# Kernel optimization log

Measured on AMD Instinct MI355X. Metric: run time of the kernel, lower is better.

The kernel has to match this reference:

```python
import jax, jax.numpy as jnp
import numpy as np

N, E = 8000, 128000
IN_DIM = OUT_DIM = REL_DIM = 64
NUM_RELS, NUM_BASES = 200, 50
R2 = 2 * NUM_RELS


def setup_inputs() -> dict:
    key = jax.random.key(0)
    ks = jax.random.split(key, 10)
    feat = jax.random.normal(ks[0], (N, IN_DIM), jnp.float32)
    rel_emb = jax.random.normal(ks[1], (R2, REL_DIM), jnp.float32)
    weight = jax.random.normal(ks[2], (NUM_BASES, IN_DIM, OUT_DIM), jnp.float32) * 0.05
    w_comp = jax.random.normal(ks[3], (R2, NUM_BASES), jnp.float32) * 0.1
    self_loop_weight = jax.random.normal(ks[4], (IN_DIM, OUT_DIM), jnp.float32) * 0.05
    W_R_w = jax.random.normal(ks[5], (REL_DIM, REL_DIM), jnp.float32) * 0.05
    W_R_b = jnp.zeros((REL_DIM,), jnp.float32)
    src = jax.random.randint(ks[6], (E,), 0, N, dtype=jnp.int32)
    dst = jax.random.randint(ks[7], (E,), 0, N, dtype=jnp.int32)
    etype = jax.random.randint(ks[8], (E,), 0, R2, dtype=jnp.int32)
    return dict(feat=feat, rel_emb=rel_emb, weight=weight, w_comp=w_comp,
                self_loop_weight=self_loop_weight, W_R_w=W_R_w, W_R_b=W_R_b,
                src=src, dst=dst, etype=etype)


def reference(feat, rel_emb, weight, w_comp, self_loop_weight, W_R_w, W_R_b,
              src, dst, etype):
    # rel_weight = (w_comp @ weight.view(B, in*out)).view(R2, in, out)
    rel_weight = jnp.einsum('rb,bio->rio', w_comp, weight)          # [R2, in, out]
    # msg_func: per-edge relation weight gather + bmm (gather-mm pattern)
    w_e = rel_weight[etype]                                          # [E, in, out]
    msg = jnp.einsum('ei,eio->eo', feat[src], w_e)                   # [E, out]
    # aggregator: alpha = 1/in_deg(dst) per edge -> weighted sum == mean over mailbox
    ones = jnp.ones((msg.shape[0],), msg.dtype)
    in_deg = jax.ops.segment_sum(ones, dst, num_segments=N)          # [N]
    nei_sum = jax.ops.segment_sum(msg, dst, num_segments=N)          # [N, out]
    nei_msg = nei_sum / jnp.maximum(in_deg, 1.0)[:, None]
    # curr_emb = dst_feat @ self_loop_weight (same for every edge into a node)
    curr_emb = feat @ self_loop_weight                               # [N, out]
    h = curr_emb + nei_msg                                           # no bias / no activation
    # is_input_layer=True: repr = cat([feat, h])
    repr_ = jnp.concatenate([feat, h], axis=1)                       # [N, in+out]
    # edge_update: W_R linear on relation embeddings (act is None)
    rel_emb_new = rel_emb @ W_R_w.T + W_R_b                          # [R2, rel_dim]
    return repr_, rel_emb_new
```

## Files before the change

### kernel.cpp

```cpp
#include <hip/hip_runtime.h>

#define N_NODES 8000
#define E_EDGES 128000
#define NUM_BASES 50
#define R2 400
#define CPR 8
#define RT 16
#define HB 32
#define EPB (E_EDGES / HB)

static __device__ __forceinline__ float bf2f(unsigned short u) {
    return __uint_as_float(((unsigned int)u) << 16);
}
static __device__ __forceinline__ unsigned short f2bf(float f) {
    unsigned int u = __float_as_uint(f);
    u += 0x7fffu + ((u >> 16) & 1u);
    return (unsigned short)(u >> 16);
}
static __device__ __forceinline__ float bcast(float v, int lane) {
    return __uint_as_float(__builtin_amdgcn_readlane(__float_as_uint(v), lane));
}

__global__ __launch_bounds__(256) void k_zero(int4* __restrict__ p, int n4) {
    const int i = blockIdx.x * 256 + threadIdx.x;
    if (i < n4) p[i] = make_int4(0, 0, 0, 0);
}

__global__ __launch_bounds__(256) void k_pre(const float* __restrict__ w_comp,
                                             const float* __restrict__ weight,
                                             unsigned short* __restrict__ relWh,
                                             const int* __restrict__ dst,
                                             const int* __restrict__ etype,
                                             int* __restrict__ bcnt,
                                             int* __restrict__ dcnt16) {
    const int blk = blockIdx.x;
    const int t = threadIdx.x;
    if (blk < 100) {
        const int rt = blk >> 2;
        const int pb = blk & 3;
        const int r0 = rt * RT;
        const int p = pb * 256 + t;
        const float4* w4 = (const float4*)weight;
        float4 acc[RT];
#pragma unroll
        for (int rr = 0; rr < RT; ++rr) acc[rr] = make_float4(0.f, 0.f, 0.f, 0.f);
        for (int b = 0; b < NUM_BASES; ++b) {
            const float4 w = w4[b * 1024 + p];
#pragma unroll
            for (int rr = 0; rr < RT; ++rr) {
                const float c = w_comp[(r0 + rr) * NUM_BASES + b];
                acc[rr].x = fmaf(c, w.x, acc[rr].x);
                acc[rr].y = fmaf(c, w.y, acc[rr].y);
                acc[rr].z = fmaf(c, w.z, acc[rr].z);
                acc[rr].w = fmaf(c, w.w, acc[rr].w);
            }
        }
        ushort4* outh = (ushort4*)relWh;
#pragma unroll
        for (int rr = 0; rr < RT; ++rr) {
            ushort4 v;
            v.x = f2bf(acc[rr].x); v.y = f2bf(acc[rr].y);
            v.z = f2bf(acc[rr].z); v.w = f2bf(acc[rr].w);
            outh[(r0 + rr) * 1024 + p] = v;
        }
    } else {
        __shared__ int lcnt[R2];
        const int hb = blk - 100;
        for (int i = t; i < R2; i += 256) lcnt[i] = 0;
        __syncthreads();
        const int e0 = hb * EPB;
        for (int e = e0 + t; e < e0 + EPB; e += 256) {
            atomicAdd(&lcnt[etype[e]], 1);
            atomicAdd(&dcnt16[dst[e] * 16], 1);
        }
        __syncthreads();
        for (int i = t; i < R2; i += 256) bcnt[hb * R2 + i] = lcnt[i];
    }
}

__global__ __launch_bounds__(512) void k_scan(const int* __restrict__ bcnt,
                                              const int* __restrict__ dcnt16,
                                              int* __restrict__ off,
                                              int* __restrict__ doff,
                                              int* __restrict__ bbase,
                                              int* __restrict__ dcursor16) {
    __shared__ int sh[8];
    const int t = threadIdx.x;
    const int lane = t & 63;
    const int wid = t >> 6;
    if (blockIdx.x == 0) {
        int tot = 0;
        if (t < R2)
            for (int b = 0; b < HB; ++b) tot += bcnt[b * R2 + t];
        int v = tot;
#pragma unroll
        for (int d = 1; d < 64; d <<= 1) {
            const int u = __shfl_up(v, d, 64);
            if (lane >= d) v += u;
        }
        if (lane == 63) sh[wid] = v;
        __syncthreads();
        int wo = 0;
        for (int i = 0; i < wid; ++i) wo += sh[i];
        const int incl = v + wo;
        const int ex = incl - tot;
        if (t == 0) off[0] = 0;
        if (t < R2) {
            off[t + 1] = incl;
            int run = ex;
            for (int b = 0; b < HB; ++b) {
                bbase[b * R2 + t] = run;
                run += bcnt[b * R2 + t];
            }
        }
    } else {
        int loc[32];
        int run = 0;
        const int base = t * 32;
        if (t < 256) {
#pragma unroll
            for (int q = 0; q < 32; ++q) {
                const int v = (base + q < N_NODES) ? dcnt16[(base + q) * 16] : 0;
                loc[q] = run;
                run += v;
            }
        }
        int v = (t < 256) ? run : 0;
#pragma unroll
        for (int d = 1; d < 64; d <<= 1) {
            const int u = __shfl_up(v, d, 64);
            if (lane >= d) v += u;
        }
        if (lane == 63 && wid < 4) sh[wid] = v;
        __syncthreads();
        if (t < 256) {
            int wo = 0;
            for (int i = 0; i < wid; ++i) wo += sh[i];
            const int incl = v + wo;
            const int ex = incl - run;
#pragma unroll
            for (int q = 0; q < 32; ++q) {
                if (base + q < N_NODES) {
                    const int o = ex + loc[q];
                    doff[base + q] = o;
                    dcursor16[(base + q) * 16] = o;
                }
            }
            if (t == 255) doff[N_NODES] = incl;
        }
    }
}

__global__ __launch_bounds__(256) void k_scatter(const int* __restrict__ src,
                                                 const int* __restrict__ dst,
                                                 const int* __restrict__ etype,
                                                 const int* __restrict__ bbase,
                                                 int* __restrict__ dcursor16,
                                                 int2* __restrict__ sedge) {
    __shared__ int lcur[R2];
    const int blk = blockIdx.x;
    const int t = threadIdx.x;
    for (int i = t; i < R2; i += 256) lcur[i] = bbase[blk * R2 + i];
    __syncthreads();
    const int e0 = blk * EPB;
    for (int e = e0 + t; e < e0 + EPB; e += 256) {
        const int r = etype[e];
        const int d = dst[e];
        const int rpos = atomicAdd(&lcur[r], 1);
        const int dpos = atomicAdd(&dcursor16[d * 16], 1);
        sedge[rpos] = make_int2(src[e], dpos);
    }
}

__global__ __launch_bounds__(64, 1) void k_edge(const float* __restrict__ feat,
                                                const unsigned short* __restrict__ relWh,
                                                const int2* __restrict__ sedge,
                                                const int* __restrict__ off,
                                                unsigned short* __restrict__ msg) {
    const int blk = blockIdx.x;
    const int xcd = blk & 7;
    const int j = blk >> 3;
    const int r = xcd * 50 + (j >> 3);
    const int chunk = j & 7;
    const int lane = threadIdx.x;
    const int beg = off[r];
    const int cnt = off[r + 1] - beg;
    const int cbeg = beg + (cnt * chunk) / CPR;
    const int cend = beg + (cnt * (chunk + 1)) / CPR;

    const unsigned short* __restrict__ Wh = relWh + r * 4096;
    float w[64];
#pragma unroll
    for (int i = 0; i < 64; ++i) w[i] = bf2f(Wh[i * 64 + lane]);

    int idx = cbeg;
    for (; idx + 1 < cend; idx += 2) {
        const int2 eA = sedge[idx];
        const int2 eB = sedge[idx + 1];
        const int sA = __builtin_amdgcn_readfirstlane(eA.x);
        const int dA = __builtin_amdgcn_readfirstlane(eA.y);
        const int sB = __builtin_amdgcn_readfirstlane(eB.x);
        const int dB = __builtin_amdgcn_readfirstlane(eB.y);
        const float* __restrict__ fA = feat + sA * 64;
        const float* __restrict__ fB = feat + sB * 64;
        float a0 = 0.f, a1 = 0.f, a2 = 0.f, a3 = 0.f;
        float b0 = 0.f, b1 = 0.f, b2 = 0.f, b3 = 0.f;
#pragma unroll
        for (int i = 0; i < 64; i += 4) {
            a0 = fmaf(fA[i    ], w[i    ], a0);  b0 = fmaf(fB[i    ], w[i    ], b0);
            a1 = fmaf(fA[i + 1], w[i + 1], a1);  b1 = fmaf(fB[i + 1], w[i + 1], b1);
            a2 = fmaf(fA[i + 2], w[i + 2], a2);  b2 = fmaf(fB[i + 2], w[i + 2], b2);
            a3 = fmaf(fA[i + 3], w[i + 3], a3);  b3 = fmaf(fB[i + 3], w[i + 3], b3);
        }
        msg[dA * 64 + lane] = f2bf((a0 + a1) + (a2 + a3));
        msg[dB * 64 + lane] = f2bf((b0 + b1) + (b2 + b3));
    }
    if (idx < cend) {
        const int2 eA = sedge[idx];
        const int sA = __builtin_amdgcn_readfirstlane(eA.x);
        const int dA = __builtin_amdgcn_readfirstlane(eA.y);
        const float* __restrict__ frow = feat + sA * 64;
        float a0 = 0.f, a1 = 0.f, a2 = 0.f, a3 = 0.f;
#pragma unroll
        for (int i = 0; i < 64; i += 4) {
            a0 = fmaf(frow[i    ], w[i    ], a0);
            a1 = fmaf(frow[i + 1], w[i + 1], a1);
            a2 = fmaf(frow[i + 2], w[i + 2], a2);
            a3 = fmaf(frow[i + 3], w[i + 3], a3);
        }
        msg[dA * 64 + lane] = f2bf((a0 + a1) + (a2 + a3));
    }
}

__global__ __launch_bounds__(256) void k_post(const float* __restrict__ feat,
                                              const float* __restrict__ slw,
                                              const int* __restrict__ doff,
                                              const unsigned short* __restrict__ msg,
                                              const float* __restrict__ rel_emb,
                                              const float* __restrict__ Wr,
                                              const float* __restrict__ br,
                                              float* __restrict__ out) {
    __shared__ float s_w[4096];
    const int blk = blockIdx.x;
    const int t = threadIdx.x;
    const int lane = t & 63;
    const int wv = t >> 6;
    if (blk < 500) {
#pragma unroll
        for (int k = 0; k < 16; ++k) s_w[k * 256 + t] = slw[k * 256 + t];
        __syncthreads();
#pragma unroll
        for (int q = 0; q < 4; ++q) {
            const int n = blk * 16 + wv * 4 + q;
            const int b0 = doff[n];
            const int b1 = doff[n + 1];
            const float* __restrict__ frow = feat + n * 64;
            const float fa = frow[lane];
            float acc = 0.f;
#pragma unroll
            for (int i = 0; i < 64; ++i)
                acc = fmaf(frow[i], s_w[i * 64 + lane], acc);
            float sm = 0.f;
            int jj = b0;
            for (; jj + 3 < b1; jj += 4) {
                const float m0 = bf2f(msg[jj * 64 + lane]);
                const float m1 = bf2f(msg[(jj + 1) * 64 + lane]);
                const float m2 = bf2f(msg[(jj + 2) * 64 + lane]);
                const float m3 = bf2f(msg[(jj + 3) * 64 + lane]);
                sm += (m0 + m1) + (m2 + m3);
            }
            for (; jj < b1; ++jj) sm += bf2f(msg[jj * 64 + lane]);
            const float inv = 1.0f / fmaxf((float)(b1 - b0), 1.0f);
            out[n * 128 + lane] = fa;
            out[n * 128 + 64 + lane] = fmaf(sm, inv, acc);
        }
    } else {
#pragma unroll
        for (int k = 0; k < 16; ++k) {
            const int idx = k * 256 + t;
            s_w[(idx & 63) * 64 + (idx >> 6)] = Wr[idx];
        }
        __syncthreads();
        const int r = (blk - 500) * 4 + wv;
        const float re = rel_emb[r * 64 + lane];
        float acc = br[lane];
#pragma unroll
        for (int k = 0; k < 64; ++k)
            acc = fmaf(bcast(re, k), s_w[k * 64 + lane], acc);
        out[N_NODES * 128 + r * 64 + lane] = acc;
    }
}

extern "C" void kernel_launch(void* const* d_in, const int* in_sizes, int n_in,
                              void* d_out, int out_size, void* d_ws, size_t ws_size,
                              hipStream_t stream) {
    const float* feat    = (const float*)d_in[0];
    const float* rel_emb = (const float*)d_in[1];
    const float* weight  = (const float*)d_in[2];
    const float* w_comp  = (const float*)d_in[3];
    const float* slw     = (const float*)d_in[4];
    const float* Wr      = (const float*)d_in[5];
    const float* br      = (const float*)d_in[6];
    const int*   src     = (const int*)d_in[7];
    const int*   dst     = (const int*)d_in[8];
    const int*   etype   = (const int*)d_in[9];
    float* out = (float*)d_out;
    char* ws = (char*)d_ws;

    unsigned short* relWh   = (unsigned short*)(ws);
    unsigned short* msg     = (unsigned short*)(ws + 3276800);
    int2* sedge     = (int2*)(ws + 19660800);
    int* off        = (int*)(ws + 20684800);
    int* doff       = (int*)(ws + 20686464);
    int* bcnt       = (int*)(ws + 20718528);
    int* bbase      = (int*)(ws + 20769728);
    int* dcnt16     = (int*)(ws + 20820928);
    int* dcursor16  = (int*)(ws + 21332928);

    k_zero<<<125, 256, 0, stream>>>((int4*)dcnt16, 32000);
    k_pre<<<132, 256, 0, stream>>>(w_comp, weight, relWh, dst, etype,
                                   bcnt, dcnt16);
    k_scan<<<2, 512, 0, stream>>>(bcnt, dcnt16, off, doff, bbase, dcursor16);
    k_scatter<<<HB, 256, 0, stream>>>(src, dst, etype, bbase, dcursor16, sedge);
    k_edge<<<R2 * CPR, 64, 0, stream>>>(feat, relWh, sedge, off, msg);
    k_post<<<600, 256, 0, stream>>>(feat, slw, doff, msg, rel_emb, Wr, br, out);
}
```

Before: 117.1 us.

## Replace global dst-count atomics with per-block shared histograms and parallel scan

Destination in-degree counting and the cursor used for placing edges into dst-sorted order now run on per-block shared-memory histograms (64 blocks × 8000 nodes) instead of padded global atomics. The zero-fill kernel is removed. The single-block node scan becomes a 250-block scan that uses a global atomic cursor to hand out node bases, so node segments are laid out in arbitrary order, with per-node counts stored explicitly for the post kernel. This targets global atomic contention and the serial scan bottleneck, at the cost of more workspace traffic for the 64×8000 count and base arrays.

```diff
diff --git a/kernel.cpp b/kernel.cpp
--- a/kernel.cpp
+++ b/kernel.cpp
@@ -4,10 +4,10 @@
 #define E_EDGES 128000
 #define NUM_BASES 50
 #define R2 400
+#define HB 64
+#define EPB (E_EDGES / HB)
+#define RT 16
 #define CPR 8
-#define RT 16
-#define HB 32
-#define EPB (E_EDGES / HB)
 
 static __device__ __forceinline__ float bf2f(unsigned short u) {
     return __uint_as_float(((unsigned int)u) << 16);
@@ -16,14 +16,6 @@
     unsigned int u = __float_as_uint(f);
     u += 0x7fffu + ((u >> 16) & 1u);
     return (unsigned short)(u >> 16);
-}
-static __device__ __forceinline__ float bcast(float v, int lane) {
-    return __uint_as_float(__builtin_amdgcn_readlane(__float_as_uint(v), lane));
-}
-
-__global__ __launch_bounds__(256) void k_zero(int4* __restrict__ p, int n4) {
-    const int i = blockIdx.x * 256 + threadIdx.x;
-    if (i < n4) p[i] = make_int4(0, 0, 0, 0);
 }
 
 __global__ __launch_bounds__(256) void k_pre(const float* __restrict__ w_comp,
@@ -32,10 +24,13 @@
                                              const int* __restrict__ dst,
                                              const int* __restrict__ etype,
                                              int* __restrict__ bcnt,
-                                             int* __restrict__ dcnt16) {
+                                             int* __restrict__ dbcnt,
+                                             int* __restrict__ gcur) {
+    __shared__ int lcnt[8400];
     const int blk = blockIdx.x;
     const int t = threadIdx.x;
     if (blk < 100) {
+        if (blk == 0 && t == 0) gcur[0] = 0;
         const int rt = blk >> 2;
         const int pb = blk & 3;
         const int r0 = rt * RT;
@@ -64,89 +59,95 @@
             outh[(r0 + rr) * 1024 + p] = v;
         }
     } else {
-        __shared__ int lcnt[R2];
-        const int hb = blk - 100;
-        for (int i = t; i < R2; i += 256) lcnt[i] = 0;
-        __syncthreads();
-        const int e0 = hb * EPB;
+        const int h = blk - 100;
+        for (int i = t; i < 8400; i += 256) lcnt[i] = 0;
+        __syncthreads();
+        const int e0 = h * EPB;
         for (int e = e0 + t; e < e0 + EPB; e += 256) {
-            atomicAdd(&lcnt[etype[e]], 1);
-            atomicAdd(&dcnt16[dst[e] * 16], 1);
-        }
-        __syncthreads();
-        for (int i = t; i < R2; i += 256) bcnt[hb * R2 + i] = lcnt[i];
-    }
-}
-
-__global__ __launch_bounds__(512) void k_scan(const int* __restrict__ bcnt,
-                                              const int* __restrict__ dcnt16,
+            atomicAdd(&lcnt[dst[e]], 1);
+            atomicAdd(&lcnt[8000 + etype[e]], 1);
+        }
+        __syncthreads();
+        for (int i = t; i < 8000; i += 256) dbcnt[h * 8000 + i] = lcnt[i];
+        for (int i = t; i < 400; i += 256) bcnt[h * 400 + i] = lcnt[8000 + i];
+    }
+}
+
+__global__ __launch_bounds__(256) void k_scan(const int* __restrict__ bcnt,
+                                              const int* __restrict__ dbcnt,
                                               int* __restrict__ off,
                                               int* __restrict__ doff,
+                                              int* __restrict__ dtot,
                                               int* __restrict__ bbase,
-                                              int* __restrict__ dcursor16) {
-    __shared__ int sh[8];
+                                              int* __restrict__ dbase,
+                                              int* __restrict__ gcur) {
     const int t = threadIdx.x;
     const int lane = t & 63;
-    const int wid = t >> 6;
-    if (blockIdx.x == 0) {
+    const int wv = t >> 6;
+    if (blockIdx.x < 250) {
+        __shared__ int T[64 * 32];
+        __shared__ int sdoff[32];
+        __shared__ int sbase;
+        const int n0 = blockIdx.x * 32;
+#pragma unroll
+        for (int pass = 0; pass < 8; ++pass) {
+            const int row = pass * 8 + (t >> 5);
+            const int col = t & 31;
+            T[row * 32 + col] = dbcnt[row * 8000 + n0 + col];
+        }
+        __syncthreads();
         int tot = 0;
-        if (t < R2)
-            for (int b = 0; b < HB; ++b) tot += bcnt[b * R2 + t];
-        int v = tot;
-#pragma unroll
-        for (int d = 1; d < 64; d <<= 1) {
-            const int u = __shfl_up(v, d, 64);
-            if (lane >= d) v += u;
-        }
-        if (lane == 63) sh[wid] = v;
-        __syncthreads();
-        int wo = 0;
-        for (int i = 0; i < wid; ++i) wo += sh[i];
-        const int incl = v + wo;
-        const int ex = incl - tot;
-        if (t == 0) off[0] = 0;
-        if (t < R2) {
-            off[t + 1] = incl;
-            int run = ex;
-            for (int b = 0; b < HB; ++b) {
-                bbase[b * R2 + t] = run;
-                run += bcnt[b * R2 + t];
-            }
+        if (t < 32) {
+            for (int hb = 0; hb < 64; ++hb) tot += T[hb * 32 + t];
+        }
+        int v = (t < 64) ? tot : 0;
+        if (t < 64) {
+#pragma unroll
+            for (int d = 1; d < 64; d <<= 1) {
+                const int u = __shfl_up(v, d, 64);
+                if (lane >= d) v += u;
+            }
+        }
+        if (t == 31) sbase = atomicAdd(gcur, v);
+        __syncthreads();
+        if (t < 32) {
+            const int dn = sbase + v - tot;
+            doff[n0 + t] = dn;
+            dtot[n0 + t] = tot;
+            sdoff[t] = dn;
+        }
+        __syncthreads();
+        for (int nl = wv; nl < 32; nl += 4) {
+            const int orig = T[lane * 32 + nl];
+            int s = orig;
+#pragma unroll
+            for (int d = 1; d < 64; d <<= 1) {
+                const int u = __shfl_up(s, d, 64);
+                if (lane >= d) s += u;
+            }
+            dbase[lane * 8000 + n0 + nl] = sdoff[nl] + s - orig;
         }
     } else {
-        int loc[32];
-        int run = 0;
-        const int base = t * 32;
-        if (t < 256) {
-#pragma unroll
-            for (int q = 0; q < 32; ++q) {
-                const int v = (base + q < N_NODES) ? dcnt16[(base + q) * 16] : 0;
-                loc[q] = run;
-                run += v;
-            }
-        }
-        int v = (t < 256) ? run : 0;
-#pragma unroll
-        for (int d = 1; d < 64; d <<= 1) {
-            const int u = __shfl_up(v, d, 64);
-            if (lane >= d) v += u;
-        }
-        if (lane == 63 && wid < 4) sh[wid] = v;
-        __syncthreads();
-        if (t < 256) {
-            int wo = 0;
-            for (int i = 0; i < wid; ++i) wo += sh[i];
-            const int incl = v + wo;
-            const int ex = incl - run;
-#pragma unroll
-            for (int q = 0; q < 32; ++q) {
-                if (base + q < N_NODES) {
-                    const int o = ex + loc[q];
-                    doff[base + q] = o;
-                    dcursor16[(base + q) * 16] = o;
-                }
-            }
-            if (t == 255) doff[N_NODES] = incl;
+        __shared__ int s[800];
+        for (int r = t; r < 400; r += 256) {
+            int sum = 0;
+            for (int hb = 0; hb < HB; ++hb) sum += bcnt[hb * 400 + r];
+            s[r] = sum;
+        }
+        __syncthreads();
+        if (t == 0) {
+            int run = 0;
+            for (int r = 0; r < 400; ++r) { s[400 + r] = run; run += s[r]; }
+            off[0] = 0;
+        }
+        __syncthreads();
+        for (int r = t; r < 400; r += 256) {
+            int run = s[400 + r];
+            off[r + 1] = run + s[r];
+            for (int hb = 0; hb < HB; ++hb) {
+                bbase[hb * 400 + r] = run;
+                run += bcnt[hb * 400 + r];
+            }
         }
     }
 }
@@ -155,19 +156,20 @@
                                                  const int* __restrict__ dst,
                                                  const int* __restrict__ etype,
                                                  const int* __restrict__ bbase,
-                                                 int* __restrict__ dcursor16,
+                                                 const int* __restrict__ dbase,
                                                  int2* __restrict__ sedge) {
-    __shared__ int lcur[R2];
-    const int blk = blockIdx.x;
+    __shared__ int cur[8400];
+    const int h = blockIdx.x;
     const int t = threadIdx.x;
-    for (int i = t; i < R2; i += 256) lcur[i] = bbase[blk * R2 + i];
+    for (int i = t; i < 8000; i += 256) cur[i] = dbase[h * 8000 + i];
+    for (int i = t; i < 400; i += 256) cur[8000 + i] = bbase[h * 400 + i];
     __syncthreads();
-    const int e0 = blk * EPB;
+    const int e0 = h * EPB;
     for (int e = e0 + t; e < e0 + EPB; e += 256) {
         const int r = etype[e];
         const int d = dst[e];
-        const int rpos = atomicAdd(&lcur[r], 1);
-        const int dpos = atomicAdd(&dcursor16[d * 16], 1);
+        const int rpos = atomicAdd(&cur[8000 + r], 1);
+        const int dpos = atomicAdd(&cur[d], 1);
         sedge[rpos] = make_int2(src[e], dpos);
     }
 }
@@ -178,9 +180,9 @@
                                                 const int* __restrict__ off,
                                                 unsigned short* __restrict__ msg) {
     const int blk = blockIdx.x;
-    const int xcd = blk & 7;
+    const int band = blk & 7;
     const int j = blk >> 3;
-    const int r = xcd * 50 + (j >> 3);
+    const int r = band * 50 + (j >> 3);
     const int chunk = j & 7;
     const int lane = threadIdx.x;
     const int beg = off[r];
@@ -235,6 +237,7 @@
 __global__ __launch_bounds__(256) void k_post(const float* __restrict__ feat,
                                               const float* __restrict__ slw,
                                               const int* __restrict__ doff,
+                                              const int* __restrict__ dtot,
                                               const unsigned short* __restrict__ msg,
                                               const float* __restrict__ rel_emb,
                                               const float* __restrict__ Wr,
@@ -253,7 +256,7 @@
         for (int q = 0; q < 4; ++q) {
             const int n = blk * 16 + wv * 4 + q;
             const int b0 = doff[n];
-            const int b1 = doff[n + 1];
+            const int b1 = b0 + dtot[n];
             const float* __restrict__ frow = feat + n * 64;
             const float fa = frow[lane];
             float acc = 0.f;
@@ -282,11 +285,11 @@
         }
         __syncthreads();
         const int r = (blk - 500) * 4 + wv;
-        const float re = rel_emb[r * 64 + lane];
+        const float* __restrict__ rrow = rel_emb + r * 64;
         float acc = br[lane];
 #pragma unroll
         for (int k = 0; k < 64; ++k)
-            acc = fmaf(bcast(re, k), s_w[k * 64 + lane], acc);
+            acc = fmaf(rrow[k], s_w[k * 64 + lane], acc);
         out[N_NODES * 128 + r * 64 + lane] = acc;
     }
 }
@@ -307,21 +310,24 @@
     float* out = (float*)d_out;
     char* ws = (char*)d_ws;
 
-    unsigned short* relWh   = (unsigned short*)(ws);
-    unsigned short* msg     = (unsigned short*)(ws + 3276800);
-    int2* sedge     = (int2*)(ws + 19660800);
-    int* off        = (int*)(ws + 20684800);
-    int* doff       = (int*)(ws + 20686464);
-    int* bcnt       = (int*)(ws + 20718528);
-    int* bbase      = (int*)(ws + 20769728);
-    int* dcnt16     = (int*)(ws + 20820928);
-    int* dcursor16  = (int*)(ws + 21332928);
-
-    k_zero<<<125, 256, 0, stream>>>((int4*)dcnt16, 32000);
-    k_pre<<<132, 256, 0, stream>>>(w_comp, weight, relWh, dst, etype,
-                                   bcnt, dcnt16);
-    k_scan<<<2, 512, 0, stream>>>(bcnt, dcnt16, off, doff, bbase, dcursor16);
-    k_scatter<<<HB, 256, 0, stream>>>(src, dst, etype, bbase, dcursor16, sedge);
+    unsigned short* relWh = (unsigned short*)(ws);
+    unsigned short* msg   = (unsigned short*)(ws + 3276800);
+    int2* sedge  = (int2*)(ws + 19660800);
+    int* off     = (int*)(ws + 20684800);
+    int* doff    = (int*)(ws + 20686464);
+    int* dtot    = (int*)(ws + 20718464);
+    int* bcnt    = (int*)(ws + 20750464);
+    int* bbase   = (int*)(ws + 20852864);
+    int* dbcnt   = (int*)(ws + 20955264);
+    int* dbase   = (int*)(ws + 23003264);
+    int* gcur    = (int*)(ws + 25051264);
+
+    k_pre<<<164, 256, 0, stream>>>(w_comp, weight, relWh, dst, etype,
+                                   bcnt, dbcnt, gcur);
+    k_scan<<<251, 256, 0, stream>>>(bcnt, dbcnt, off, doff, dtot,
+                                    bbase, dbase, gcur);
+    k_scatter<<<HB, 256, 0, stream>>>(src, dst, etype, bbase, dbase, sedge);
     k_edge<<<R2 * CPR, 64, 0, stream>>>(feat, relWh, sedge, off, msg);
-    k_post<<<600, 256, 0, stream>>>(feat, slw, doff, msg, rel_emb, Wr, br, out);
-}
+    k_post<<<600, 256, 0, stream>>>(feat, slw, doff, dtot, msg,
+                                    rel_emb, Wr, br, out);
+}
```

New measurement: 110.2 us. -5.9%, faster.
